# Optimization experiments

Measured on AMD Instinct MI355X. Metric: run time of the kernel, lower is better.

The kernel has to match this reference:

```python
import jax, jax.numpy as jnp
import numpy as np

D_MODEL = 1024
N_HEADS = 16
D_K = D_MODEL // N_HEADS
B, T = 2, 2048


def setup_inputs() -> dict:
    key = jax.random.key(0)
    ks = jax.random.split(key, 12)
    s = 0.02
    return {
        "q": jax.random.normal(ks[0], (B, T, D_MODEL), jnp.float32),
        "k": jax.random.normal(ks[1], (B, T, D_MODEL), jnp.float32),
        "v": jax.random.normal(ks[2], (B, T, D_MODEL), jnp.float32),
        "Wq": jax.random.normal(ks[3], (D_MODEL, D_MODEL), jnp.float32) * s,
        "bq": jnp.zeros((D_MODEL,), jnp.float32),
        "Wk": jax.random.normal(ks[4], (D_MODEL, D_MODEL), jnp.float32) * s,
        "bk": jnp.zeros((D_MODEL,), jnp.float32),
        "Wv": jax.random.normal(ks[5], (D_MODEL, D_MODEL), jnp.float32) * s,
        "bv": jnp.zeros((D_MODEL,), jnp.float32),
        "Wo": jax.random.normal(ks[6], (D_MODEL, D_MODEL), jnp.float32) * s,
        "bo": jnp.zeros((D_MODEL,), jnp.float32),
        "mask": jnp.ones((B, T), jnp.int32),
        "causal": 1,
    }


def reference(q, k, v, Wq, bq, Wk, bk, Wv, bv, Wo, bo, mask, causal):
    Bq, Tq, D = q.shape
    Tk = k.shape[1]
    # projections (torch Linear: x @ W.T + b), split heads -> [B, H, T, d_k]
    qh = (q @ Wq.T + bq).reshape(Bq, Tq, N_HEADS, D_K).transpose(0, 2, 1, 3)
    kh = (k @ Wk.T + bk).reshape(Bq, Tk, N_HEADS, D_K).transpose(0, 2, 1, 3)
    vh = (v @ Wv.T + bv).reshape(Bq, Tk, N_HEADS, D_K).transpose(0, 2, 1, 3)
    scores = jnp.einsum("bhqd,bhkd->bhqk", qh, kh) / jnp.sqrt(jnp.float32(D_K))
    neg_inf = jnp.float32(-jnp.inf)
    if mask is not None:
        scores = jnp.where(mask[:, None, None, :] == 0, neg_inf, scores)
    if causal:
        causal_mask = jnp.tril(jnp.ones((Tq, Tq), jnp.float32))
        scores = jnp.where(causal_mask == 0, neg_inf, scores)
    attn = jax.nn.softmax(scores, axis=-1)
    out = jnp.einsum("bhqk,bhkd->bhqd", attn, vh)
    out = out.transpose(0, 2, 1, 3).reshape(Bq, Tq, D)
    return out @ Wo.T + bo
```

## Files before the change

kernel.cpp:

```cpp
#include <hip/hip_runtime.h>
#include <cstdint>
#include <cstddef>


typedef __bf16 bf16x8 __attribute__((ext_vector_type(8)));
typedef float f32x4 __attribute__((ext_vector_type(4)));

#define MFMA(a, b, c) __builtin_amdgcn_mfma_f32_16x16x32_bf16((a), (b), (c), 0, 0, 0)

static constexpr int D_MODEL = 1024;
static constexpr int T_ = 2048;
static constexpr int M_TOK = 4096;

__device__ __forceinline__ unsigned short f32_to_bf16(float f) {
    union { float f; uint32_t u; } v; v.f = f;
    uint32_t u = v.u;
    uint32_t r = u + 0x7fffu + ((u >> 16) & 1u);
    return (unsigned short)(r >> 16);
}
__device__ __forceinline__ unsigned pk2(float a, float b) {
    union { __bf16 h[2]; unsigned u; } z;
    z.h[0] = (__bf16)a; z.h[1] = (__bf16)b;
    return z.u;
}

typedef __attribute__((address_space(1))) void* as1_ptr;
typedef __attribute__((address_space(3))) void* as3_ptr;
__device__ __forceinline__ void gload_lds16(const void* g, void* l) {
    __builtin_amdgcn_global_load_lds((as1_ptr)(void*)g, (as3_ptr)l, 16, 0, 0);
}

__device__ __forceinline__ int keyperm(int k) {
    return (k & 32) | ((k & 12) << 1) | ((k & 16) >> 2) | (k & 3);
}

__global__ __launch_bounds__(256) void cvt_all(
    const float* __restrict__ q, const float* __restrict__ k,
    const float* __restrict__ v, const float* __restrict__ wq,
    const float* __restrict__ wk, const float* __restrict__ wv,
    const float* __restrict__ wo, ushort4* __restrict__ dst) {
    int i = blockIdx.x * blockDim.x + threadIdx.x;
    constexpr int R = 1 << 20;
    const float* s;
    int idx;
    if (i < 3 * R) {
        s = (i < R) ? q : (i < 2 * R) ? k : v;
        idx = i & (R - 1);
    } else {
        int j = i - 3 * R;
        int w = j >> 18;
        s = (w == 0) ? wq : (w == 1) ? wk : (w == 2) ? wv : wo;
        idx = j & ((1 << 18) - 1);
    }
    float4 f = ((const float4*)s)[idx];
    ushort4 o;
    o.x = (unsigned short)f32_to_bf16(f.x); o.y = (unsigned short)f32_to_bf16(f.y);
    o.z = (unsigned short)f32_to_bf16(f.z); o.w = (unsigned short)f32_to_bf16(f.w);
    dst[i] = o;
}

template<int MODE, int NT16>
__device__ __forceinline__ void gemm_body(
    const unsigned short* __restrict__ A, const unsigned short* __restrict__ W,
    const float* __restrict__ bias, void* __restrict__ outp,
    unsigned short* As, unsigned short* Ws, int bx, int by, float oscale)
{
    constexpr bool SWAP = (MODE != 2);
    constexpr int BKE = 32;
    constexpr int ASZ = 128 * BKE;
    constexpr int WSZ = NT16 * 32 * BKE;
    constexpr int AL = ASZ / (256 * 8);
    constexpr int WL = WSZ / (256 * 8);
    constexpr int NKS = D_MODEL / BKE;
    const int tid = threadIdx.x;
    const int lane = tid & 63, wave = tid >> 6;
    const int wm = wave >> 1, wn = wave & 1;
    const int r16 = lane & 15, kg = lane >> 4;
    const int m_blk = by * 128, n_blk = bx * (NT16 * 32);

    const unsigned short* Ap[AL]; unsigned short* Albase[AL];
    #pragma unroll
    for (int j = 0; j < AL; ++j) {
        int si = j * 256 + tid;
        int row = si >> 2, p = si & 3, g = p ^ ((row >> 1) & 3);
        Ap[j] = A + (size_t)(m_blk + row) * D_MODEL + g * 8;
        Albase[j] = As + (j * 256 + wave * 64) * 8;
    }
    const unsigned short* Wp[WL]; unsigned short* Wlbase[WL];
    #pragma unroll
    for (int j = 0; j < WL; ++j) {
        int si = j * 256 + tid;
        int row = si >> 2, p = si & 3, g = p ^ ((row >> 1) & 3);
        Wp[j] = W + (size_t)(n_blk + row) * D_MODEL + g * 8;
        Wlbase[j] = Ws + (j * 256 + wave * 64) * 8;
    }

    int aoff[4], woff[NT16];
    #pragma unroll
    for (int mt = 0; mt < 4; ++mt) {
        int row = wm * 64 + mt * 16 + r16;
        aoff[mt] = row * BKE + ((kg ^ ((row >> 1) & 3)) * 8);
    }
    #pragma unroll
    for (int nt = 0; nt < NT16; ++nt) {
        int row = wn * (NT16 * 16) + nt * 16 + r16;
        woff[nt] = row * BKE + ((kg ^ ((row >> 1) & 3)) * 8);
    }

    f32x4 acc[4][NT16];
    #pragma unroll
    for (int mt = 0; mt < 4; ++mt)
        #pragma unroll
        for (int nt = 0; nt < NT16; ++nt) acc[mt][nt] = (f32x4){0, 0, 0, 0};

    auto stage = [&](int bb, int k0) {
        #pragma unroll
        for (int j = 0; j < AL; ++j)
            gload_lds16(Ap[j] + k0, Albase[j] + bb * ASZ);
        #pragma unroll
        for (int j = 0; j < WL; ++j)
            gload_lds16(Wp[j] + k0, Wlbase[j] + bb * WSZ);
    };

    stage(0, 0);
    stage(1, BKE);
    int cb = 0;
    for (int ks = 0; ks < NKS; ++ks) {
        if (ks + 1 < NKS) asm volatile("s_waitcnt vmcnt(4)" ::: "memory");
        else              asm volatile("s_waitcnt vmcnt(0)" ::: "memory");
        __builtin_amdgcn_s_barrier();
        __builtin_amdgcn_sched_barrier(0);
        if (ks + 2 < NKS) {
            int sb = cb + 2; if (sb >= 3) sb -= 3;
            stage(sb, (ks + 2) * BKE);
        }
        const unsigned short* Asb = As + cb * ASZ;
        const unsigned short* Wsb = Ws + cb * WSZ;
        bf16x8 af[4], wf[NT16];
        #pragma unroll
        for (int mt = 0; mt < 4; ++mt)
            af[mt] = *(const bf16x8*)(Asb + aoff[mt]);
        #pragma unroll
        for (int nt = 0; nt < NT16; ++nt)
            wf[nt] = *(const bf16x8*)(Wsb + woff[nt]);
        #pragma unroll
        for (int mt = 0; mt < 4; ++mt)
            #pragma unroll
            for (int nt = 0; nt < NT16; ++nt)
                acc[mt][nt] = SWAP ? MFMA(wf[nt], af[mt], acc[mt][nt])
                                   : MFMA(af[mt], wf[nt], acc[mt][nt]);
        cb = (cb == 2) ? 0 : cb + 1;
    }

    if (MODE == 2) {
        #pragma unroll
        for (int nt = 0; nt < NT16; ++nt) {
            int n = n_blk + wn * (NT16 * 16) + nt * 16 + r16;
            float bn = bias[n];
            int hh = n >> 6, dki = n & 63;
            #pragma unroll
            for (int mt = 0; mt < 4; ++mt) {
                int m0 = m_blk + wm * 64 + mt * 16 + kg * 4;
                int mp = (m0 & ~63) | keyperm(m0 & 63);
                int bb = mp >> 11, ti = mp & 2047;
                ushort4 pk;
                pk.x = f32_to_bf16((acc[mt][nt][0] + bn) * oscale);
                pk.y = f32_to_bf16((acc[mt][nt][1] + bn) * oscale);
                pk.z = f32_to_bf16((acc[mt][nt][2] + bn) * oscale);
                pk.w = f32_to_bf16((acc[mt][nt][3] + bn) * oscale);
                *(ushort4*)((unsigned short*)outp +
                    ((size_t)(bb * 16 + hh) * 64 + dki) * 2048 + ti) = pk;
            }
        }
    } else {
        #pragma unroll
        for (int nt = 0; nt < NT16; ++nt) {
            int n0 = n_blk + wn * (NT16 * 16) + nt * 16 + kg * 4;
            float4 bn4 = *(const float4*)(bias + n0);
            #pragma unroll
            for (int mt = 0; mt < 4; ++mt) {
                int m = m_blk + wm * 64 + mt * 16 + r16;
                if (MODE == 3) {
                    float4 st;
                    st.x = (acc[mt][nt][0] + bn4.x) * oscale;
                    st.y = (acc[mt][nt][1] + bn4.y) * oscale;
                    st.z = (acc[mt][nt][2] + bn4.z) * oscale;
                    st.w = (acc[mt][nt][3] + bn4.w) * oscale;
                    *(float4*)((float*)outp + (size_t)m * D_MODEL + n0) = st;
                } else {
                    ushort4 pk;
                    pk.x = f32_to_bf16((acc[mt][nt][0] + bn4.x) * oscale);
                    pk.y = f32_to_bf16((acc[mt][nt][1] + bn4.y) * oscale);
                    pk.z = f32_to_bf16((acc[mt][nt][2] + bn4.z) * oscale);
                    pk.w = f32_to_bf16((acc[mt][nt][3] + bn4.w) * oscale);
                    *(ushort4*)((unsigned short*)outp + (size_t)m * D_MODEL + n0) = pk;
                }
            }
        }
    }
}

__global__ __launch_bounds__(256) void gemm_qkv(
    const unsigned short* __restrict__ qb, const unsigned short* __restrict__ kb,
    const unsigned short* __restrict__ vb, const unsigned short* __restrict__ Wqb,
    const unsigned short* __restrict__ Wkb, const unsigned short* __restrict__ Wvb,
    const float* __restrict__ bq, const float* __restrict__ bk, const float* __restrict__ bv,
    unsigned short* __restrict__ Qhp, unsigned short* __restrict__ Khp,
    unsigned short* __restrict__ Vtp)
{
    __shared__ __align__(16) unsigned short As[3 * 128 * 32];
    __shared__ __align__(16) unsigned short Ws[3 * 128 * 32];
    int flat = blockIdx.x + (blockIdx.y << 3) + (blockIdx.z << 8);
    int w = (flat & 7) * 96 + (flat >> 3);
    int bx = w & 7, by = (w >> 3) & 31, z = w >> 8;
    const unsigned short* A = (z == 0) ? qb : (z == 1) ? kb : vb;
    const unsigned short* W = (z == 0) ? Wqb : (z == 1) ? Wkb : Wvb;
    const float* bias = (z == 0) ? bq : (z == 1) ? bk : bv;
    float osc = (z == 0) ? 0.18033688011112042f : 1.0f;
    if (z < 2)
        gemm_body<0, 4>(A, W, bias, (z == 0) ? (void*)Qhp : (void*)Khp, As, Ws,
                        bx, by, osc);
    else
        gemm_body<2, 4>(A, W, bias, (void*)Vtp, As, Ws, bx, by, 1.0f);
}

__global__ __launch_bounds__(256) void gemm_out(
    const unsigned short* __restrict__ ab, const unsigned short* __restrict__ Wob,
    const float* __restrict__ bo, float* __restrict__ outp)
{
    __shared__ __align__(16) unsigned short As[3 * 128 * 32];
    __shared__ __align__(16) unsigned short Ws[3 * 128 * 32];
    int flat = blockIdx.x + (blockIdx.y << 3);
    int w = (flat & 7) * 32 + (flat >> 3);
    int bx = w & 7, by = w >> 3;
    gemm_body<3, 4>(ab, Wob, bo, (void*)outp, As, Ws, bx, by, 1.0f);
}

__global__ __launch_bounds__(256) void attn_fwd(
    const unsigned short* __restrict__ Qh, const unsigned short* __restrict__ Kh,
    const unsigned short* __restrict__ Vt, const int* __restrict__ mask,
    const int* __restrict__ causal_p, unsigned short* __restrict__ attnout)
{
    __shared__ __align__(16) unsigned short Ks[3][64 * 64];
    __shared__ __align__(16) unsigned short Vs[2][64 * 64];

    const int tid = threadIdx.x;
    const int lane = tid & 63, wave = tid >> 6;
    const int bh = blockIdx.x;
    const int y = blockIdx.y, y0 = y & 7, j4 = y >> 3;
    const int qc = (j4 == 0) ? (31 - y0) : (j4 == 1) ? (16 + y0)
                 : (j4 == 2) ? (15 - y0) : y0;
    const int b = bh >> 4, h = bh & 15;
    const int causal = *causal_p;
    const int r16 = lane & 15, kg = lane >> 4;

    const int q0 = qc * 64 + wave * 16;

    const unsigned short* Qb = Qh + (size_t)b * T_ * D_MODEL + h * 64;
    const unsigned short* Kb = Kh + (size_t)b * T_ * D_MODEL + h * 64;
    const unsigned short* Vb = Vt + (size_t)bh * 64 * T_;
    const int* mb = mask + b * T_;

    const int nT = causal ? (qc + 1) : 32;

    unsigned allm = 0;
    for (int tt = 0; tt < nT; ++tt) {
        unsigned long long m = __ballot(mb[tt * 64 + lane] != 0);
        if (m == ~0ull) allm |= (1u << tt);
    }

    bf16x8 qf0 = *(const bf16x8*)(Qb + (size_t)(q0 + r16) * D_MODEL + kg * 8);
    bf16x8 qf1 = *(const bf16x8*)(Qb + (size_t)(q0 + r16) * D_MODEL + 32 + kg * 8);

    union { unsigned u[4]; bf16x8 v; } onef;
    onef.u[0] = onef.u[1] = onef.u[2] = onef.u[3] = 0x3f803f80u;

    f32x4 lacc = (f32x4){0, 0, 0, 0};
    f32x4 o[4];
    #pragma unroll
    for (int f = 0; f < 4; ++f) o[f] = (f32x4){0, 0, 0, 0};
    const int lim = wave * 16 + r16;

    const unsigned short* Kp[2]; const unsigned short* Vp[2];
    char* Kl[2]; char* Vl[2];
    #pragma unroll
    for (int j = 0; j < 2; ++j) {
        int si = j * 256 + tid;
        int row = si >> 3, cg = (si & 7) ^ (row & 7);
        Kp[j] = Kb + (size_t)row * D_MODEL + cg * 8;
        Vp[j] = Vb + (size_t)row * T_ + cg * 8;
        Kl[j] = (char*)Ks[0] + (j * 256 + wave * 64) * 16;
        Vl[j] = (char*)Vs[0] + (j * 256 + wave * 64) * 16;
    }
    auto stageK = [&](int buf, int t) {
        #pragma unroll
        for (int j = 0; j < 2; ++j)
            gload_lds16(Kp[j] + ((size_t)t << 16), Kl[j] + buf * 8192);
    };
    auto stageV = [&](int buf, int t) {
        #pragma unroll
        for (int j = 0; j < 2; ++j)
            gload_lds16(Vp[j] + (t << 6), Vl[j] + buf * 8192);
    };

#define TILE_ITER(KB, VB)                                                      \
    {                                                                          \
        if (t + 1 < nT) asm volatile("s_waitcnt vmcnt(2)" ::: "memory");       \
        else            asm volatile("s_waitcnt vmcnt(0)" ::: "memory");       \
        __builtin_amdgcn_s_barrier();                                          \
        __builtin_amdgcn_sched_barrier(0);                                     \
        if (t + 1 < nT) stageV(((VB) + 1) & 1, t + 1);            \
        if (t + 2 < nT) stageK(((KB) + 2) % 3, t + 2);            \
        const unsigned short* Kst = Ks[KB];                                    \
        const unsigned short* Vst = Vs[VB];                                    \
        const bool diag = causal && (t == qc);                                 \
        f32x4 s[4];                                                            \
        __builtin_amdgcn_s_setprio(1);                                         \
        _Pragma("unroll")                                                      \
        for (int c = 0; c < 4; ++c) {                                          \
            int key = c * 16 + r16;                                            \
            bf16x8 kf0 = *(const bf16x8*)(Kst + key * 64 + ((kg ^ (key & 7)) * 8));       \
            bf16x8 kf1 = *(const bf16x8*)(Kst + key * 64 + (((4 + kg) ^ (key & 7)) * 8)); \
            f32x4 z = (f32x4){0, 0, 0, 0};                                     \
            z = MFMA(kf0, qf0, z);                                             \
            z = MFMA(kf1, qf1, z);                                             \
            s[c] = z;                                                          \
        }                                                                      \
        __builtin_amdgcn_s_setprio(0);                                         \
        float pv[4][4];                                                        \
        if (!diag && ((allm >> t) & 1)) {                                      \
            _Pragma("unroll")                                                  \
            for (int c = 0; c < 4; ++c)                                        \
                _Pragma("unroll")                                              \
                for (int r = 0; r < 4; ++r)                                    \
                    pv[c][r] = __builtin_amdgcn_exp2f(s[c][r]);                \
        } else {                                                               \
            unsigned long long km = __ballot(mb[t * 64 + lane] != 0);          \
            _Pragma("unroll")                                                  \
            for (int c = 0; c < 4; ++c) {                                      \
                unsigned mc = (unsigned)(km >> (c * 16));                      \
                _Pragma("unroll")                                              \
                for (int r = 0; r < 4; ++r) {                                  \
                    int kbit = kg * 4 + r;                                     \
                    bool ok = ((mc >> kbit) & 1) && (!diag || (c * 16 + kbit <= lim)); \
                    pv[c][r] = ok ? __builtin_amdgcn_exp2f(s[c][r]) : 0.f;     \
                }                                                              \
            }                                                                  \
        }                                                                      \
        union pk_t { unsigned u[4]; bf16x8 v; };                               \
        pk_t pa[2];                                                            \
        _Pragma("unroll")                                                      \
        for (int c = 0; c < 4; ++c) {                                          \
            int half = (c & 1) * 2;                                            \
            pa[c >> 1].u[half]     = pk2(pv[c][0], pv[c][1]);                  \
            pa[c >> 1].u[half + 1] = pk2(pv[c][2], pv[c][3]);                  \
        }                                                                      \
        __builtin_amdgcn_s_setprio(1);                                         \
        lacc = MFMA(pa[0].v, onef.v, lacc);                                    \
        lacc = MFMA(pa[1].v, onef.v, lacc);                                    \
        _Pragma("unroll")                                                      \
        for (int f = 0; f < 4; ++f) {                                          \
            int row = f * 16 + r16;                                            \
            int rx = row & 7;                                                  \
            _Pragma("unroll")                                                  \
            for (int cp = 0; cp < 2; ++cp) {                                   \
                int g = cp * 4 + kg;                                           \
                bf16x8 vf = *(const bf16x8*)(Vst + row * 64 + ((g ^ rx) * 8)); \
                o[f] = MFMA(pa[cp].v, vf, o[f]);                               \
            }                                                                  \
        }                                                                      \
        __builtin_amdgcn_s_setprio(0);                                         \
    }

    stageK(0, 0);
    stageV(0, 0);
    stageK(1, 1);
    __syncthreads();
    int t = 0;
    while (t + 6 <= nT) {
        TILE_ITER(0, 0); ++t;
        TILE_ITER(1, 1); ++t;
        TILE_ITER(2, 0); ++t;
        TILE_ITER(0, 1); ++t;
        TILE_ITER(1, 0); ++t;
        TILE_ITER(2, 1); ++t;
    }
    {
        int kb = 0;
        for (; t < nT; ++t) {
            TILE_ITER(kb, t & 1);
            kb = (kb == 2) ? 0 : kb + 1;
        }
    }
#undef TILE_ITER

    #pragma unroll
    for (int r = 0; r < 4; ++r) {
        float iv = (lacc[r] > 0.f) ? 1.0f / lacc[r] : 0.f;
        size_t base = ((size_t)(b * T_ + q0 + kg * 4 + r)) * D_MODEL + h * 64;
        #pragma unroll
        for (int f = 0; f < 4; ++f)
            attnout[base + f * 16 + r16] = f32_to_bf16(o[f][r] * iv);
    }
}

extern "C" void kernel_launch(void* const* d_in, const int* in_sizes, int n_in,
                              void* d_out, int out_size, void* d_ws, size_t ws_size,
                              hipStream_t stream) {
    const float* q  = (const float*)d_in[0];
    const float* k  = (const float*)d_in[1];
    const float* v  = (const float*)d_in[2];
    const float* Wq = (const float*)d_in[3];
    const float* bq = (const float*)d_in[4];
    const float* Wk = (const float*)d_in[5];
    const float* bk = (const float*)d_in[6];
    const float* Wv = (const float*)d_in[7];
    const float* bv = (const float*)d_in[8];
    const float* Wo = (const float*)d_in[9];
    const float* bo = (const float*)d_in[10];
    const int* mask   = (const int*)d_in[11];
    const int* causal = (const int*)d_in[12];

    const size_t SZ_TOK = (size_t)M_TOK * D_MODEL;
    const size_t SZ_W   = (size_t)D_MODEL * D_MODEL;

    unsigned short* qb  = (unsigned short*)d_ws;
    unsigned short* kb  = qb  + SZ_TOK;
    unsigned short* vb  = kb  + SZ_TOK;
    unsigned short* Wqb = vb  + SZ_TOK;
    unsigned short* Wkb = Wqb + SZ_W;
    unsigned short* Wvb = Wkb + SZ_W;
    unsigned short* Wob = Wvb + SZ_W;
    unsigned short* Qhp = Wob + SZ_W;
    unsigned short* Khp = Qhp + SZ_TOK;
    unsigned short* Vtp = Khp + SZ_TOK;
    unsigned short* ab  = Vtp + SZ_TOK;

    cvt_all<<<16384, 256, 0, stream>>>(q, k, v, Wq, Wk, Wv, Wo, (ushort4*)qb);

    gemm_qkv<<<dim3(D_MODEL / 128, M_TOK / 128, 3), 256, 0, stream>>>(
        qb, kb, vb, Wqb, Wkb, Wvb, bq, bk, bv, Qhp, Khp, Vtp);

    attn_fwd<<<dim3(32, 32), 256, 0, stream>>>(Qhp, Khp, Vtp, mask, causal, ab);

    gemm_out<<<dim3(D_MODEL / 128, M_TOK / 128), 256, 0, stream>>>(ab, Wob, bo,
                                                                   (float*)d_out);
}
```

Before: 216.0 us.

## Split KV range of long causal query chunks across two blocks and combine

The attention grid grows from 32 to 48 query-chunk rows. The 16 longest causal query chunks are each split into two blocks, and each block processes half of the key tiles. Split blocks write unnormalized fp32 partial outputs and row sums to scratch space that reuses the already-consumed bf16 input buffers. A new attn_combine kernel adds the two halves and normalizes. The aim is to even out per-block work and raise occupancy on the causal triangle, at the cost of an extra launch and extra global traffic for the partials.

```diff
diff --git a/kernel.cpp b/kernel.cpp
--- a/kernel.cpp
+++ b/kernel.cpp
@@ -239,7 +239,8 @@
 __global__ __launch_bounds__(256) void attn_fwd(
     const unsigned short* __restrict__ Qh, const unsigned short* __restrict__ Kh,
     const unsigned short* __restrict__ Vt, const int* __restrict__ mask,
-    const int* __restrict__ causal_p, unsigned short* __restrict__ attnout)
+    const int* __restrict__ causal_p, unsigned short* __restrict__ attnout,
+    float* __restrict__ Opart, float* __restrict__ Lpart)
 {
     __shared__ __align__(16) unsigned short Ks[3][64 * 64];
     __shared__ __align__(16) unsigned short Vs[2][64 * 64];
@@ -247,12 +248,21 @@
     const int tid = threadIdx.x;
     const int lane = tid & 63, wave = tid >> 6;
     const int bh = blockIdx.x;
-    const int y = blockIdx.y, y0 = y & 7, j4 = y >> 3;
-    const int qc = (j4 == 0) ? (31 - y0) : (j4 == 1) ? (16 + y0)
-                 : (j4 == 2) ? (15 - y0) : y0;
+    const int y = blockIdx.y;
     const int b = bh >> 4, h = bh & 15;
     const int causal = *causal_p;
     const int r16 = lane & 15, kg = lane >> 4;
+
+    int qc, t0, t1, s;  bool spl;
+    if (y < 32) {
+        spl = true; s = y & 1; qc = 31 - (y >> 1);
+        int nT = causal ? (qc + 1) : 32;
+        int hh = nT >> 1;
+        t0 = s ? hh : 0;  t1 = s ? nT : hh;
+    } else {
+        spl = false; s = 0; qc = 47 - y;
+        t0 = 0;  t1 = causal ? (qc + 1) : 32;
+    }
 
     const int q0 = qc * 64 + wave * 16;
 
@@ -261,10 +271,8 @@
     const unsigned short* Vb = Vt + (size_t)bh * 64 * T_;
     const int* mb = mask + b * T_;
 
-    const int nT = causal ? (qc + 1) : 32;
-
     unsigned allm = 0;
-    for (int tt = 0; tt < nT; ++tt) {
+    for (int tt = t0; tt < t1; ++tt) {
         unsigned long long m = __ballot(mb[tt * 64 + lane] != 0);
         if (m == ~0ull) allm |= (1u << tt);
     }
@@ -305,16 +313,16 @@
 
 #define TILE_ITER(KB, VB)                                                      \
     {                                                                          \
-        if (t + 1 < nT) asm volatile("s_waitcnt vmcnt(2)" ::: "memory");       \
+        if (t + 1 < t1) asm volatile("s_waitcnt vmcnt(2)" ::: "memory");       \
         else            asm volatile("s_waitcnt vmcnt(0)" ::: "memory");       \
         __builtin_amdgcn_s_barrier();                                          \
         __builtin_amdgcn_sched_barrier(0);                                     \
-        if (t + 1 < nT) stageV(((VB) + 1) & 1, t + 1);            \
-        if (t + 2 < nT) stageK(((KB) + 2) % 3, t + 2);            \
+        if (t + 1 < t1) stageV(((VB) + 1) & 1, t + 1);            \
+        if (t + 2 < t1) stageK(((KB) + 2) % 3, t + 2);            \
         const unsigned short* Kst = Ks[KB];                                    \
         const unsigned short* Vst = Vs[VB];                                    \
         const bool diag = causal && (t == qc);                                 \
-        f32x4 s[4];                                                            \
+        f32x4 sv[4];                                                           \
         __builtin_amdgcn_s_setprio(1);                                         \
         _Pragma("unroll")                                                      \
         for (int c = 0; c < 4; ++c) {                                          \
@@ -324,7 +332,7 @@
             f32x4 z = (f32x4){0, 0, 0, 0};                                     \
             z = MFMA(kf0, qf0, z);                                             \
             z = MFMA(kf1, qf1, z);                                             \
-            s[c] = z;                                                          \
+            sv[c] = z;                                                         \
         }                                                                      \
         __builtin_amdgcn_s_setprio(0);                                         \
         float pv[4][4];                                                        \
@@ -333,7 +341,7 @@
             for (int c = 0; c < 4; ++c)                                        \
                 _Pragma("unroll")                                              \
                 for (int r = 0; r < 4; ++r)                                    \
-                    pv[c][r] = __builtin_amdgcn_exp2f(s[c][r]);                \
+                    pv[c][r] = __builtin_amdgcn_exp2f(sv[c][r]);               \
         } else {                                                               \
             unsigned long long km = __ballot(mb[t * 64 + lane] != 0);          \
             _Pragma("unroll")                                                  \
@@ -343,7 +351,7 @@
                 for (int r = 0; r < 4; ++r) {                                  \
                     int kbit = kg * 4 + r;                                     \
                     bool ok = ((mc >> kbit) & 1) && (!diag || (c * 16 + kbit <= lim)); \
-                    pv[c][r] = ok ? __builtin_amdgcn_exp2f(s[c][r]) : 0.f;     \
+                    pv[c][r] = ok ? __builtin_amdgcn_exp2f(sv[c][r]) : 0.f;    \
                 }                                                              \
             }                                                                  \
         }                                                                      \
@@ -372,12 +380,12 @@
         __builtin_amdgcn_s_setprio(0);                                         \
     }
 
-    stageK(0, 0);
-    stageV(0, 0);
-    stageK(1, 1);
+    stageK(0, t0);
+    stageV(0, t0);
+    if (t0 + 1 < t1) stageK(1, t0 + 1);
     __syncthreads();
-    int t = 0;
-    while (t + 6 <= nT) {
+    int t = t0;
+    while (t + 6 <= t1) {
         TILE_ITER(0, 0); ++t;
         TILE_ITER(1, 1); ++t;
         TILE_ITER(2, 0); ++t;
@@ -386,21 +394,60 @@
         TILE_ITER(2, 1); ++t;
     }
     {
-        int kb = 0;
-        for (; t < nT; ++t) {
-            TILE_ITER(kb, t & 1);
+        int kb = 0, vbuf = 0;
+        for (; t < t1; ++t) {
+            TILE_ITER(kb, vbuf);
             kb = (kb == 2) ? 0 : kb + 1;
+            vbuf ^= 1;
         }
     }
 #undef TILE_ITER
 
-    #pragma unroll
-    for (int r = 0; r < 4; ++r) {
-        float iv = (lacc[r] > 0.f) ? 1.0f / lacc[r] : 0.f;
-        size_t base = ((size_t)(b * T_ + q0 + kg * 4 + r)) * D_MODEL + h * 64;
-        #pragma unroll
-        for (int f = 0; f < 4; ++f)
-            attnout[base + f * 16 + r16] = f32_to_bf16(o[f][r] * iv);
+    if (!spl) {
+        #pragma unroll
+        for (int r = 0; r < 4; ++r) {
+            float iv = (lacc[r] > 0.f) ? 1.0f / lacc[r] : 0.f;
+            size_t base = ((size_t)(b * T_ + q0 + kg * 4 + r)) * D_MODEL + h * 64;
+            #pragma unroll
+            for (int f = 0; f < 4; ++f)
+                attnout[base + f * 16 + r16] = f32_to_bf16(o[f][r] * iv);
+        }
+    } else {
+        int p = ((bh * 16 + (qc - 16)) * 2 + s);
+        float* Ob = Opart + (size_t)p * 4096;
+        float* Lb = Lpart + p * 64;
+        #pragma unroll
+        for (int r = 0; r < 4; ++r) {
+            int ql = wave * 16 + kg * 4 + r;
+            #pragma unroll
+            for (int f = 0; f < 4; ++f)
+                Ob[ql * 64 + f * 16 + r16] = o[f][r];
+            if (r16 == 0) Lb[ql] = lacc[r];
+        }
+    }
+}
+
+__global__ __launch_bounds__(256) void attn_combine(
+    const float* __restrict__ Opart, const float* __restrict__ Lpart,
+    unsigned short* __restrict__ ab)
+{
+    const int bh = blockIdx.x, qci = blockIdx.y;
+    const int b = bh >> 4, h = bh & 15;
+    const int qc = 16 + qci;
+    const int p0 = (bh * 16 + qci) * 2;
+    const float* O0 = Opart + (size_t)p0 * 4096;
+    const float* O1 = O0 + 4096;
+    const float* L0 = Lpart + p0 * 64;
+    const float* L1 = L0 + 64;
+    const int tid = threadIdx.x;
+    const int row = tid >> 2, c0 = (tid & 3) * 16;
+    float l = L0[row] + L1[row];
+    float inv = (l > 0.f) ? 1.0f / l : 0.f;
+    size_t base = ((size_t)(b * T_ + qc * 64 + row)) * D_MODEL + h * 64 + c0;
+    #pragma unroll
+    for (int j = 0; j < 16; ++j) {
+        float v = (O0[row * 64 + c0 + j] + O1[row * 64 + c0 + j]) * inv;
+        ab[base + j] = f32_to_bf16(v);
     }
 }
 
@@ -436,12 +483,18 @@
     unsigned short* Vtp = Khp + SZ_TOK;
     unsigned short* ab  = Vtp + SZ_TOK;
 
+    float* Opart = (float*)qb;
+    float* Lpart = (float*)vb;
+
     cvt_all<<<16384, 256, 0, stream>>>(q, k, v, Wq, Wk, Wv, Wo, (ushort4*)qb);
 
     gemm_qkv<<<dim3(D_MODEL / 128, M_TOK / 128, 3), 256, 0, stream>>>(
         qb, kb, vb, Wqb, Wkb, Wvb, bq, bk, bv, Qhp, Khp, Vtp);
 
-    attn_fwd<<<dim3(32, 32), 256, 0, stream>>>(Qhp, Khp, Vtp, mask, causal, ab);
+    attn_fwd<<<dim3(32, 48), 256, 0, stream>>>(Qhp, Khp, Vtp, mask, causal, ab,
+                                               Opart, Lpart);
+
+    attn_combine<<<dim3(32, 16), 256, 0, stream>>>(Opart, Lpart, ab);
 
     gemm_out<<<dim3(D_MODEL / 128, M_TOK / 128), 256, 0, stream>>>(ab, Wob, bo,
                                                                    (float*)d_out);
```

New measurement: 218.6 us. No clear change (+1.2%).

## Split attention tile across waves by query and key halves with LDS reduction

Applied to the files above, without the earlier changes.

Each of the four waves now handles 32 queries against 32 keys of each 64-key tile, where before each wave took 16 queries against all 64 keys. The two key-half partial outputs and row sums are then combined through shared memory at the end. This lets each K fragment be reused across two query groups and each V fragment across two P operands, cutting LDS reads per MFMA. It also adds launch bounds targeting 4 blocks per CU. The cost is an extra reduction pass through LDS with two barriers, and more accumulator registers, which the launch-bounds cap may squeeze.

```diff
diff --git a/kernel.cpp b/kernel.cpp
--- a/kernel.cpp
+++ b/kernel.cpp
@@ -236,7 +236,7 @@
     gemm_body<3, 4>(ab, Wob, bo, (void*)outp, As, Ws, bx, by, 1.0f);
 }
 
-__global__ __launch_bounds__(256) void attn_fwd(
+__global__ __launch_bounds__(256, 4) void attn_fwd(
     const unsigned short* __restrict__ Qh, const unsigned short* __restrict__ Kh,
     const unsigned short* __restrict__ Vt, const int* __restrict__ mask,
     const int* __restrict__ causal_p, unsigned short* __restrict__ attnout)
@@ -246,6 +246,7 @@
 
     const int tid = threadIdx.x;
     const int lane = tid & 63, wave = tid >> 6;
+    const int qh = wave & 1, kh = wave >> 1;
     const int bh = blockIdx.x;
     const int y = blockIdx.y, y0 = y & 7, j4 = y >> 3;
     const int qc = (j4 == 0) ? (31 - y0) : (j4 == 1) ? (16 + y0)
@@ -254,8 +255,6 @@
     const int causal = *causal_p;
     const int r16 = lane & 15, kg = lane >> 4;
 
-    const int q0 = qc * 64 + wave * 16;
-
     const unsigned short* Qb = Qh + (size_t)b * T_ * D_MODEL + h * 64;
     const unsigned short* Kb = Kh + (size_t)b * T_ * D_MODEL + h * 64;
     const unsigned short* Vb = Vt + (size_t)bh * 64 * T_;
@@ -269,17 +268,24 @@
         if (m == ~0ull) allm |= (1u << tt);
     }
 
-    bf16x8 qf0 = *(const bf16x8*)(Qb + (size_t)(q0 + r16) * D_MODEL + kg * 8);
-    bf16x8 qf1 = *(const bf16x8*)(Qb + (size_t)(q0 + r16) * D_MODEL + 32 + kg * 8);
+    bf16x8 qf0[2], qf1[2];
+    #pragma unroll
+    for (int g = 0; g < 2; ++g) {
+        const unsigned short* qrow =
+            Qb + (size_t)(qc * 64 + qh * 32 + g * 16 + r16) * D_MODEL;
+        qf0[g] = *(const bf16x8*)(qrow + kg * 8);
+        qf1[g] = *(const bf16x8*)(qrow + 32 + kg * 8);
+    }
 
     union { unsigned u[4]; bf16x8 v; } onef;
     onef.u[0] = onef.u[1] = onef.u[2] = onef.u[3] = 0x3f803f80u;
 
-    f32x4 lacc = (f32x4){0, 0, 0, 0};
-    f32x4 o[4];
-    #pragma unroll
-    for (int f = 0; f < 4; ++f) o[f] = (f32x4){0, 0, 0, 0};
-    const int lim = wave * 16 + r16;
+    f32x4 lacc[2] = {(f32x4){0, 0, 0, 0}, (f32x4){0, 0, 0, 0}};
+    f32x4 o[2][4];
+    #pragma unroll
+    for (int g = 0; g < 2; ++g)
+        #pragma unroll
+        for (int f = 0; f < 4; ++f) o[g][f] = (f32x4){0, 0, 0, 0};
 
     const unsigned short* Kp[2]; const unsigned short* Vp[2];
     char* Kl[2]; char* Vl[2];
@@ -314,67 +320,76 @@
         const unsigned short* Kst = Ks[KB];                                    \
         const unsigned short* Vst = Vs[VB];                                    \
         const bool diag = causal && (t == qc);                                 \
-        f32x4 s[4];                                                            \
+        f32x4 sv[2][2];                                                        \
         __builtin_amdgcn_s_setprio(1);                                         \
         _Pragma("unroll")                                                      \
-        for (int c = 0; c < 4; ++c) {                                          \
-            int key = c * 16 + r16;                                            \
+        for (int c = 0; c < 2; ++c) {                                          \
+            int key = kh * 32 + c * 16 + r16;                                  \
             bf16x8 kf0 = *(const bf16x8*)(Kst + key * 64 + ((kg ^ (key & 7)) * 8));       \
             bf16x8 kf1 = *(const bf16x8*)(Kst + key * 64 + (((4 + kg) ^ (key & 7)) * 8)); \
-            f32x4 z = (f32x4){0, 0, 0, 0};                                     \
-            z = MFMA(kf0, qf0, z);                                             \
-            z = MFMA(kf1, qf1, z);                                             \
-            s[c] = z;                                                          \
+            _Pragma("unroll")                                                  \
+            for (int g = 0; g < 2; ++g) {                                      \
+                f32x4 z = (f32x4){0, 0, 0, 0};                                 \
+                z = MFMA(kf0, qf0[g], z);                                      \
+                z = MFMA(kf1, qf1[g], z);                                      \
+                sv[c][g] = z;                                                  \
+            }                                                                  \
         }                                                                      \
         __builtin_amdgcn_s_setprio(0);                                         \
-        float pv[4][4];                                                        \
+        float pv[2][2][4];                                                     \
         if (!diag && ((allm >> t) & 1)) {                                      \
             _Pragma("unroll")                                                  \
-            for (int c = 0; c < 4; ++c)                                        \
+            for (int c = 0; c < 2; ++c)                                        \
                 _Pragma("unroll")                                              \
-                for (int r = 0; r < 4; ++r)                                    \
-                    pv[c][r] = __builtin_amdgcn_exp2f(s[c][r]);                \
+                for (int g = 0; g < 2; ++g)                                    \
+                    _Pragma("unroll")                                          \
+                    for (int r = 0; r < 4; ++r)                                \
+                        pv[c][g][r] = __builtin_amdgcn_exp2f(sv[c][g][r]);     \
         } else {                                                               \
             unsigned long long km = __ballot(mb[t * 64 + lane] != 0);          \
             _Pragma("unroll")                                                  \
-            for (int c = 0; c < 4; ++c) {                                      \
-                unsigned mc = (unsigned)(km >> (c * 16));                      \
+            for (int c = 0; c < 2; ++c) {                                      \
+                unsigned mc = (unsigned)(km >> (kh * 32 + c * 16));            \
                 _Pragma("unroll")                                              \
-                for (int r = 0; r < 4; ++r) {                                  \
-                    int kbit = kg * 4 + r;                                     \
-                    bool ok = ((mc >> kbit) & 1) && (!diag || (c * 16 + kbit <= lim)); \
-                    pv[c][r] = ok ? __builtin_amdgcn_exp2f(s[c][r]) : 0.f;     \
+                for (int g = 0; g < 2; ++g) {                                  \
+                    int limg = qh * 32 + g * 16 + r16;                         \
+                    _Pragma("unroll")                                          \
+                    for (int r = 0; r < 4; ++r) {                              \
+                        int kbit = kg * 4 + r;                                 \
+                        int klim = kh * 32 + c * 16 + kbit;                    \
+                        bool ok = ((mc >> kbit) & 1) && (!diag || (klim <= limg)); \
+                        pv[c][g][r] = ok ? __builtin_amdgcn_exp2f(sv[c][g][r]) : 0.f; \
+                    }                                                          \
                 }                                                              \
             }                                                                  \
         }                                                                      \
         union pk_t { unsigned u[4]; bf16x8 v; };                               \
         pk_t pa[2];                                                            \
         _Pragma("unroll")                                                      \
-        for (int c = 0; c < 4; ++c) {                                          \
-            int half = (c & 1) * 2;                                            \
-            pa[c >> 1].u[half]     = pk2(pv[c][0], pv[c][1]);                  \
-            pa[c >> 1].u[half + 1] = pk2(pv[c][2], pv[c][3]);                  \
-        }                                                                      \
+        for (int g = 0; g < 2; ++g)                                            \
+            _Pragma("unroll")                                                  \
+            for (int c = 0; c < 2; ++c) {                                      \
+                pa[g].u[c * 2]     = pk2(pv[c][g][0], pv[c][g][1]);            \
+                pa[g].u[c * 2 + 1] = pk2(pv[c][g][2], pv[c][g][3]);            \
+            }                                                                  \
         __builtin_amdgcn_s_setprio(1);                                         \
-        lacc = MFMA(pa[0].v, onef.v, lacc);                                    \
-        lacc = MFMA(pa[1].v, onef.v, lacc);                                    \
+        lacc[0] = MFMA(pa[0].v, onef.v, lacc[0]);                              \
+        lacc[1] = MFMA(pa[1].v, onef.v, lacc[1]);                              \
         _Pragma("unroll")                                                      \
         for (int f = 0; f < 4; ++f) {                                          \
             int row = f * 16 + r16;                                            \
             int rx = row & 7;                                                  \
-            _Pragma("unroll")                                                  \
-            for (int cp = 0; cp < 2; ++cp) {                                   \
-                int g = cp * 4 + kg;                                           \
-                bf16x8 vf = *(const bf16x8*)(Vst + row * 64 + ((g ^ rx) * 8)); \
-                o[f] = MFMA(pa[cp].v, vf, o[f]);                               \
-            }                                                                  \
+            int gg = kh * 4 + kg;           \
+            bf16x8 vf = *(const bf16x8*)(Vst + row * 64 + ((gg ^ rx) * 8));    \
+            o[0][f] = MFMA(pa[0].v, vf, o[0][f]);                              \
+            o[1][f] = MFMA(pa[1].v, vf, o[1][f]);                              \
         }                                                                      \
         __builtin_amdgcn_s_setprio(0);                                         \
     }
 
     stageK(0, 0);
     stageV(0, 0);
-    stageK(1, 1);
+    if (nT > 1) stageK(1, 1);
     __syncthreads();
     int t = 0;
     while (t + 6 <= nT) {
@@ -386,21 +401,49 @@
         TILE_ITER(2, 1); ++t;
     }
     {
-        int kb = 0;
+        int kb = 0, vbuf = 0;
         for (; t < nT; ++t) {
-            TILE_ITER(kb, t & 1);
+            TILE_ITER(kb, vbuf);
             kb = (kb == 2) ? 0 : kb + 1;
+            vbuf ^= 1;
         }
     }
 #undef TILE_ITER
 
-    #pragma unroll
-    for (int r = 0; r < 4; ++r) {
-        float iv = (lacc[r] > 0.f) ? 1.0f / lacc[r] : 0.f;
-        size_t base = ((size_t)(b * T_ + q0 + kg * 4 + r)) * D_MODEL + h * 64;
-        #pragma unroll
-        for (int f = 0; f < 4; ++f)
-            attnout[base + f * 16 + r16] = f32_to_bf16(o[f][r] * iv);
+    __syncthreads();
+    float* sm = (float*)Ks;
+    float* lsm = sm + 2 * 2176;
+    if (kh == 1) {
+        #pragma unroll
+        for (int g = 0; g < 2; ++g) {
+            #pragma unroll
+            for (int r = 0; r < 4; ++r) {
+                int row = g * 16 + kg * 4 + r;
+                #pragma unroll
+                for (int f = 0; f < 4; ++f)
+                    sm[qh * 2176 + row * 68 + f * 16 + r16] = o[g][f][r];
+                if (r16 == 0) lsm[qh * 32 + row] = lacc[g][r];
+            }
+        }
+    }
+    __syncthreads();
+    if (kh == 0) {
+        #pragma unroll
+        for (int g = 0; g < 2; ++g) {
+            #pragma unroll
+            for (int r = 0; r < 4; ++r) {
+                int row = g * 16 + kg * 4 + r;
+                float l = lacc[g][r] + lsm[qh * 32 + row];
+                float iv = (l > 0.f) ? 1.0f / l : 0.f;
+                size_t base = ((size_t)(b * T_ + qc * 64 + qh * 32 + row))
+                              * D_MODEL + h * 64;
+                #pragma unroll
+                for (int f = 0; f < 4; ++f) {
+                    float v = o[g][f][r] + sm[qh * 2176 + row * 68 + f * 16 + r16];
+                    attnout[base + f * 16 + r16] = f32_to_bf16(v * iv);
+                }
+            }
+        }
     }
 }
 
```

Result: no change. 219.8 us (+1.8%).
